# Kernel optimization log

Hardware: AMD Instinct MI355X
Metric: run time of the kernel (lower is better)

## Reference

```python
import jax, jax.numpy as jnp
import numpy as np

T, B, D, H = 110, 256, 512, 512
EPS = 1e-9


def _forward(a, v, l, qmask, umask, mu_a, mu_v, mu_l, shifta, shiftv,
             turna, turnb, W1, b1, W2, b2):
    Tcur = a.shape[0]
    # ca = mu * (cos(a) + i sin(a)) = mu * exp(i a)
    ca = mu_a[:Tcur] * jnp.exp(1j * a)          # (T,B,D) complex64
    cv = mu_v[:Tcur] * jnp.exp(1j * v)
    cl = mu_l[:Tcur] * jnp.exp(1j * l)
    # phase shift of a and v streams, then sum into lav
    features = cl + ca * jnp.exp(1j * shifta) + cv * jnp.exp(1j * shiftv)  # (T,B,D)

    # --- step 0 (special-cased in the original loop) ---
    temp0 = features[0]                          # (B,D) complex
    qa0 = qmask[0][:, 0:1]                       # (B,1)
    qb0 = qmask[0][:, 1:2]
    ones = jnp.ones_like(temp0) * (1.0 + 1.0j)   # pA=pB=1+1j initial state
    pA0 = (1.0 - qa0) * ones + qa0 * temp0
    pB0 = (1.0 - qb0) * ones + qb0 * temp0

    # --- steps 1..T-1 as a fused scan over time ---
    def step(carry, xs):
        pA, pB = carry
        f, qm, ta, tb = xs                       # f:(B,D) cplx, qm:(B,2), ta/tb:(1,D)
        qa = qm[:, 0:1]
        qb = qm[:, 1:2]
        turn = qa * (pA * jnp.exp(1j * ta)) + qb * (pB * jnp.exp(1j * tb))
        # torch: turn.where(turn==0, turn/(abs+eps)) -> keep 0 where 0, else normalize
        turn = jnp.where(turn == 0, turn, turn / (jnp.abs(turn) + EPS))
        temp = f + turn
        pA = (1.0 - qa) * pA + qa * temp
        pB = (1.0 - qb) * pB + qb * temp
        return (pA, pB), temp

    (_, _), temps = jax.lax.scan(
        step, (pA0, pB0),
        (features[1:], qmask[1:], turna[1:Tcur], turnb[1:Tcur]))

    feats = jnp.concatenate([temp0[None], temps], axis=0)  # (T,B,D) complex
    fr, fi = feats.real, feats.imag
    f1r = fr @ W1.T + b1
    f1i = fi @ W1.T + b1
    f2r = fr @ W2.T + b2
    f2i = fi @ W2.T + b2
    xr = f1r - f2i
    xi = f1i + f2r
    return xr + xi                               # (T,B,H) float32


def setup_inputs() -> dict:
    key = jax.random.key(0)
    ks = jax.random.split(key, 12)
    a = jax.random.normal(ks[0], (T, B, D), jnp.float32)
    v = jax.random.normal(ks[1], (T, B, D), jnp.float32)
    l = jax.random.normal(ks[2], (T, B, D), jnp.float32)
    spk = jax.random.randint(ks[3], (T, B), 0, 2)
    qmask = jax.nn.one_hot(spk, 2, dtype=jnp.float32)      # (T,B,2)
    umask = jnp.ones((T, B), jnp.float32)                  # unused by forward
    mu_a = jnp.ones((110, 1, 1), jnp.float32)
    mu_v = jnp.ones((110, 1, 1), jnp.float32)
    mu_l = jnp.ones((110, 1, 1), jnp.float32)
    shifta = jax.random.normal(ks[4], (1, 1, D), jnp.float32)
    shiftv = jax.random.normal(ks[5], (1, 1, D), jnp.float32)
    turna = jax.random.uniform(ks[6], (110, 1, D), jnp.float32)
    turnb = jax.random.uniform(ks[7], (110, 1, D), jnp.float32)
    W1 = jax.random.normal(ks[8], (H, D), jnp.float32) * 0.02
    b1 = jnp.zeros((H,), jnp.float32)
    W2 = jax.random.normal(ks[9], (H, D), jnp.float32) * 0.02
    b2 = jnp.zeros((H,), jnp.float32)
    return {"a": a, "v": v, "l": l, "qmask": qmask, "umask": umask,
            "mu_a": mu_a, "mu_v": mu_v, "mu_l": mu_l,
            "shifta": shifta, "shiftv": shiftv,
            "turna": turna, "turnb": turnb,
            "W1": W1, "b1": b1, "W2": W2, "b2": b2,
            "dia_len": T}


def reference(a, v, l, qmask, umask, mu_a, mu_v, mu_l, shifta, shiftv,
              turna, turnb, W1, b1, W2, b2, dia_len):
    return _forward(a, v, l, qmask, umask, mu_a, mu_v, mu_l,
                    shifta, shiftv, turna, turnb, W1, b1, W2, b2)
```

## Files before the change

### kernel.cpp

```cpp
#include <hip/hip_runtime.h>

#define T_DIM 110
#define B_DIM 256
#define D_DIM 512
#define H_DIM 512
#define K_CAT 1024
#define M_DIM (T_DIM * B_DIM)
#define BD    (B_DIM * D_DIM)
#define EPSV 1e-9f

typedef float f32x4 __attribute__((ext_vector_type(4)));
typedef short bf16x8 __attribute__((ext_vector_type(8)));

static __device__ __forceinline__ unsigned short f2bf(float f) {
    unsigned u = __builtin_bit_cast(unsigned, f);
    u += 0x7fffu + ((u >> 16) & 1u);
    return (unsigned short)(u >> 16);
}

__global__ __launch_bounds__(256) void prep_w_kernel(
    const float* __restrict__ W1, const float* __restrict__ b1,
    const float* __restrict__ W2,
    unsigned short* __restrict__ Bt,
    float* __restrict__ bias2)
{
    int i = blockIdx.x * 256 + threadIdx.x;
    if (i < H_DIM) bias2[i] = 2.0f * b1[i];
    if (i >= H_DIM * K_CAT) return;
    int h = i / K_CAT;
    int k = i % K_CAT;
    float w;
    if (k < D_DIM) w = W1[h * D_DIM + k] + W2[h * D_DIM + k];
    else           w = W1[h * D_DIM + k - D_DIM] - W2[h * D_DIM + k - D_DIM];
    Bt[i] = f2bf(w);
}

__global__ __launch_bounds__(256) void feat_scan_kernel(
    const float* __restrict__ a, const float* __restrict__ v,
    const float* __restrict__ l, const float* __restrict__ qmask,
    const float* __restrict__ mu_a, const float* __restrict__ mu_v,
    const float* __restrict__ mu_l,
    const float* __restrict__ shifta, const float* __restrict__ shiftv,
    const float* __restrict__ turna, const float* __restrict__ turnb,
    unsigned short* __restrict__ A)
{
    const int tid = blockIdx.x * blockDim.x + threadIdx.x;
    const int b = tid >> 9;
    const int d = tid & 511;
    const float sa = shifta[d];
    const float sv = shiftv[d];

    float a0,v0,l0,ta0,tb0,q0,ma0,mv0,ml0;
    float a1,v1,l1,ta1,tb1,q1,ma1,mv1,ml1;
    float a2,v2,l2,ta2,tb2,q2,ma2,mv2,ml2;

#define LOAD_INTO(A_,V_,L_,TA_,TB_,Q_,MA_,MV_,ML_, T_)                        \
    {                                                                          \
        const int t_ = (T_);                                                   \
        A_  = a[(size_t)t_ * BD + tid];                                        \
        V_  = v[(size_t)t_ * BD + tid];                                        \
        L_  = l[(size_t)t_ * BD + tid];                                        \
        TA_ = turna[t_ * D_DIM + d];                                           \
        TB_ = turnb[t_ * D_DIM + d];                                           \
        Q_  = qmask[(size_t)(t_ * B_DIM + b) * 2];                             \
        MA_ = mu_a[t_]; MV_ = mu_v[t_]; ML_ = mu_l[t_];                        \
    }

    LOAD_INTO(a0,v0,l0,ta0,tb0,q0,ma0,mv0,ml0, 0)
    LOAD_INTO(a1,v1,l1,ta1,tb1,q1,ma1,mv1,ml1, 1)
    LOAD_INTO(a2,v2,l2,ta2,tb2,q2,ma2,mv2,ml2, 2)

    float pAr = 0.f, pAi = 0.f, pBr = 0.f, pBi = 0.f;

    #pragma unroll 3
    for (int t = 0; t < T_DIM; ++t) {
        float an,vn,ln,tan_,tbn,qn,man,mvn,mln;
        const int tp = (t + 3 < T_DIM) ? t + 3 : T_DIM - 1;
        LOAD_INTO(an,vn,ln,tan_,tbn,qn,man,mvn,mln, tp)

        float sA, cA, sV, cV, sL, cL;
        __sincosf(a0 + sa, &sA, &cA);
        __sincosf(v0 + sv, &sV, &cV);
        __sincosf(l0,      &sL, &cL);
        float fr = ml0 * cL + ma0 * cA + mv0 * cV;
        float fi = ml0 * sL + ma0 * sA + mv0 * sV;

        const bool isA = q0 > 0.5f;
        if (t == 0) {
            pAr = isA ? fr : 1.0f;  pAi = isA ? fi : 1.0f;
            pBr = isA ? 1.0f : fr;  pBi = isA ? 1.0f : fi;
        } else {
            float ph = isA ? ta0 : tb0;
            float pr = isA ? pAr : pBr;
            float pi = isA ? pAi : pBi;
            float sp, cp;
            __sincosf(ph, &sp, &cp);
            float tr = pr * cp - pi * sp;
            float ti = pr * sp + pi * cp;
            if (!(tr == 0.0f && ti == 0.0f)) {
                float inv = 1.0f / (sqrtf(tr * tr + ti * ti) + EPSV);
                tr *= inv; ti *= inv;
            }
            fr += tr;
            fi += ti;
            if (isA) { pAr = fr; pAi = fi; } else { pBr = fr; pBi = fi; }
        }

        const size_t row = (size_t)(t * B_DIM + b) * K_CAT;
        A[row + d]         = f2bf(fr);
        A[row + D_DIM + d] = f2bf(fi);

        a0=a1; v0=v1; l0=l1; ta0=ta1; tb0=tb1; q0=q1; ma0=ma1; mv0=mv1; ml0=ml1;
        a1=a2; v1=v2; l1=l2; ta1=ta2; tb1=tb2; q1=q2; ma1=ma2; mv1=mv2; ml1=ml2;
        a2=an; v2=vn; l2=ln; ta2=tan_; tb2=tbn; q2=qn; ma2=man; mv2=mvn; ml2=mln;
    }
#undef LOAD_INTO
}

#define BM 128
#define BN 128
#define BK 32
#define LDS_PAD 40

__global__ __launch_bounds__(256) void gemm_kernel(
    const unsigned short* __restrict__ A,
    const unsigned short* __restrict__ Bt,
    const float* __restrict__ bias2,
    float* __restrict__ C)
{
    __shared__ __align__(16) unsigned short As[BM * LDS_PAD];
    __shared__ __align__(16) unsigned short Bs[BN * LDS_PAD];

    int tid = threadIdx.x;
    int wave = tid >> 6;
    int lane = tid & 63;
    int wr = wave >> 1;
    int wc = wave & 1;
    int m0 = blockIdx.x * BM;
    int n0 = blockIdx.y * BN;
    int lrow = lane & 15;
    int lk8 = (lane >> 4) * 8;

    f32x4 acc[4][4] = {};

    for (int k0 = 0; k0 < K_CAT; k0 += BK) {
        #pragma unroll
        for (int j = 0; j < 2; ++j) {
            int ch = tid + 256 * j;
            int row = ch >> 2;
            int cc = ch & 3;
            const uint4* gA = reinterpret_cast<const uint4*>(
                A + (size_t)(m0 + row) * K_CAT + k0 + cc * 8);
            *reinterpret_cast<uint4*>(&As[row * LDS_PAD + cc * 8]) = *gA;
            const uint4* gB = reinterpret_cast<const uint4*>(
                Bt + (size_t)(n0 + row) * K_CAT + k0 + cc * 8);
            *reinterpret_cast<uint4*>(&Bs[row * LDS_PAD + cc * 8]) = *gB;
        }
        __syncthreads();

        bf16x8 af[4], bfv[4];
        #pragma unroll
        for (int m = 0; m < 4; ++m)
            af[m] = *reinterpret_cast<const bf16x8*>(
                &As[(wr * 64 + m * 16 + lrow) * LDS_PAD + lk8]);
        #pragma unroll
        for (int n = 0; n < 4; ++n)
            bfv[n] = *reinterpret_cast<const bf16x8*>(
                &Bs[(wc * 64 + n * 16 + lrow) * LDS_PAD + lk8]);

        #pragma unroll
        for (int m = 0; m < 4; ++m)
            #pragma unroll
            for (int n = 0; n < 4; ++n)
                acc[m][n] = __builtin_amdgcn_mfma_f32_16x16x32_bf16(
                    af[m], bfv[n], acc[m][n], 0, 0, 0);
        __syncthreads();
    }

    int rbase = m0 + wr * 64 + (lane >> 4) * 4;
    int cbase = n0 + wc * 64;
    #pragma unroll
    for (int n = 0; n < 4; ++n) {
        int col = cbase + n * 16 + lrow;
        float bv = bias2[col];
        #pragma unroll
        for (int m = 0; m < 4; ++m) {
            int row0 = rbase + m * 16;
            #pragma unroll
            for (int r = 0; r < 4; ++r) {
                C[(size_t)(row0 + r) * H_DIM + col] = acc[m][n][r] + bv;
            }
        }
    }
}

extern "C" void kernel_launch(void* const* d_in, const int* in_sizes, int n_in,
                              void* d_out, int out_size, void* d_ws, size_t ws_size,
                              hipStream_t stream) {
    const float* a      = (const float*)d_in[0];
    const float* v      = (const float*)d_in[1];
    const float* l      = (const float*)d_in[2];
    const float* qmask  = (const float*)d_in[3];
    const float* mu_a   = (const float*)d_in[5];
    const float* mu_v   = (const float*)d_in[6];
    const float* mu_l   = (const float*)d_in[7];
    const float* shifta = (const float*)d_in[8];
    const float* shiftv = (const float*)d_in[9];
    const float* turna  = (const float*)d_in[10];
    const float* turnb  = (const float*)d_in[11];
    const float* W1     = (const float*)d_in[12];
    const float* b1     = (const float*)d_in[13];
    const float* W2     = (const float*)d_in[14];
    float* out = (float*)d_out;

    char* ws = (char*)d_ws;
    unsigned short* Afeat = (unsigned short*)ws;
    size_t offB  = (size_t)M_DIM * K_CAT * sizeof(unsigned short);
    unsigned short* Bt = (unsigned short*)(ws + offB);
    size_t offBias = offB + (size_t)H_DIM * K_CAT * sizeof(unsigned short);
    float* bias2 = (float*)(ws + offBias);

    prep_w_kernel<<<(H_DIM * K_CAT + 255) / 256, 256, 0, stream>>>(W1, b1, W2, Bt, bias2);
    feat_scan_kernel<<<(B_DIM * D_DIM) / 256, 256, 0, stream>>>(
        a, v, l, qmask, mu_a, mu_v, mu_l, shifta, shiftv, turna, turnb, Afeat);
    dim3 grid(M_DIM / BM, H_DIM / BN);
    gemm_kernel<<<grid, 256, 0, stream>>>(Afeat, Bt, bias2, out);
}
```

Before: 134.0 us.

## Use direct global-to-LDS loads with BK=64 in GEMM and pin scan prefetch registers

The GEMM now stages A and B tiles with global_load_lds (global memory straight into LDS, skipping VGPRs), doubles BK to 64 and drops the LDS row padding. Each sync now covers two MFMA k-substeps, which halves the barrier count. Empty asm register pins were added in the scan kernel so the compiler keeps the three-step prefetch loads issued early instead of sinking them. The unpadded LDS layout (row stride of 128 bytes) may cause bank conflicts on the fragment reads.

```diff
diff --git a/kernel.cpp b/kernel.cpp
--- a/kernel.cpp
+++ b/kernel.cpp
@@ -65,10 +65,15 @@
         Q_  = qmask[(size_t)(t_ * B_DIM + b) * 2];                             \
         MA_ = mu_a[t_]; MV_ = mu_v[t_]; ML_ = mu_l[t_];                        \
     }
+#define PIN6(A_,V_,L_,TA_,TB_,Q_) \
+    asm volatile("" : "+v"(A_), "+v"(V_), "+v"(L_), "+v"(TA_), "+v"(TB_), "+v"(Q_));
 
     LOAD_INTO(a0,v0,l0,ta0,tb0,q0,ma0,mv0,ml0, 0)
     LOAD_INTO(a1,v1,l1,ta1,tb1,q1,ma1,mv1,ml1, 1)
     LOAD_INTO(a2,v2,l2,ta2,tb2,q2,ma2,mv2,ml2, 2)
+    PIN6(a0,v0,l0,ta0,tb0,q0)
+    PIN6(a1,v1,l1,ta1,tb1,q1)
+    PIN6(a2,v2,l2,ta2,tb2,q2)
 
     float pAr = 0.f, pAi = 0.f, pBr = 0.f, pBi = 0.f;
 
@@ -77,6 +82,7 @@
         float an,vn,ln,tan_,tbn,qn,man,mvn,mln;
         const int tp = (t + 3 < T_DIM) ? t + 3 : T_DIM - 1;
         LOAD_INTO(an,vn,ln,tan_,tbn,qn,man,mvn,mln, tp)
+        PIN6(an,vn,ln,tan_,tbn,qn)
 
         float sA, cA, sV, cV, sL, cL;
         __sincosf(a0 + sa, &sA, &cA);
@@ -115,12 +121,12 @@
         a2=an; v2=vn; l2=ln; ta2=tan_; tb2=tbn; q2=qn; ma2=man; mv2=mvn; ml2=mln;
     }
 #undef LOAD_INTO
+#undef PIN6
 }
 
 #define BM 128
 #define BN 128
-#define BK 32
-#define LDS_PAD 40
+#define BK 64
 
 __global__ __launch_bounds__(256) void gemm_kernel(
     const unsigned short* __restrict__ A,
@@ -128,64 +134,82 @@
     const float* __restrict__ bias2,
     float* __restrict__ C)
 {
-    __shared__ __align__(16) unsigned short As[BM * LDS_PAD];
-    __shared__ __align__(16) unsigned short Bs[BN * LDS_PAD];
-
-    int tid = threadIdx.x;
-    int wave = tid >> 6;
-    int lane = tid & 63;
-    int wr = wave >> 1;
-    int wc = wave & 1;
-    int m0 = blockIdx.x * BM;
-    int n0 = blockIdx.y * BN;
-    int lrow = lane & 15;
-    int lk8 = (lane >> 4) * 8;
+    __shared__ __align__(16) unsigned short As[BM * BK];
+    __shared__ __align__(16) unsigned short Bs[BN * BK];
+
+    const int tid = threadIdx.x;
+    const int wave = tid >> 6;
+    const int lane = tid & 63;
+    const int wr = wave >> 1;
+    const int wc = wave & 1;
+    const int m0 = blockIdx.x * BM;
+    const int n0 = blockIdx.y * BN;
+    const int lrow = lane & 15;
+    const int lk8 = (lane >> 4) * 8;
+
+    const int srow = wave * 32;
+    const int lrow8 = lane >> 3;
+    const int lchunk = lane & 7;
 
     f32x4 acc[4][4] = {};
 
     for (int k0 = 0; k0 < K_CAT; k0 += BK) {
         #pragma unroll
-        for (int j = 0; j < 2; ++j) {
-            int ch = tid + 256 * j;
-            int row = ch >> 2;
-            int cc = ch & 3;
-            const uint4* gA = reinterpret_cast<const uint4*>(
-                A + (size_t)(m0 + row) * K_CAT + k0 + cc * 8);
-            *reinterpret_cast<uint4*>(&As[row * LDS_PAD + cc * 8]) = *gA;
-            const uint4* gB = reinterpret_cast<const uint4*>(
-                Bt + (size_t)(n0 + row) * K_CAT + k0 + cc * 8);
-            *reinterpret_cast<uint4*>(&Bs[row * LDS_PAD + cc * 8]) = *gB;
+        for (int c = 0; c < 4; ++c) {
+            const int row = srow + c * 8 + lrow8;
+            {
+                const unsigned short* gp = A + (size_t)(m0 + row) * K_CAT + k0 + lchunk * 8;
+                unsigned short* lp = As + (srow + c * 8) * BK + lane * 8;
+                __builtin_amdgcn_global_load_lds(
+                    (const __attribute__((address_space(1))) unsigned int*)gp,
+                    (__attribute__((address_space(3))) unsigned int*)lp,
+                    16, 0, 0);
+            }
+            {
+                const unsigned short* gp = Bt + (size_t)(n0 + row) * K_CAT + k0 + lchunk * 8;
+                unsigned short* lp = Bs + (srow + c * 8) * BK + lane * 8;
+                __builtin_amdgcn_global_load_lds(
+                    (const __attribute__((address_space(1))) unsigned int*)gp,
+                    (__attribute__((address_space(3))) unsigned int*)lp,
+                    16, 0, 0);
+            }
         }
         __syncthreads();
 
-        bf16x8 af[4], bfv[4];
+        bf16x8 af[4][2], bfv[4][2];
         #pragma unroll
         for (int m = 0; m < 4; ++m)
-            af[m] = *reinterpret_cast<const bf16x8*>(
-                &As[(wr * 64 + m * 16 + lrow) * LDS_PAD + lk8]);
+            #pragma unroll
+            for (int kk = 0; kk < 2; ++kk)
+                af[m][kk] = *reinterpret_cast<const bf16x8*>(
+                    &As[(wr * 64 + m * 16 + lrow) * BK + kk * 32 + lk8]);
         #pragma unroll
         for (int n = 0; n < 4; ++n)
-            bfv[n] = *reinterpret_cast<const bf16x8*>(
-                &Bs[(wc * 64 + n * 16 + lrow) * LDS_PAD + lk8]);
-
-        #pragma unroll
-        for (int m = 0; m < 4; ++m)
-            #pragma unroll
-            for (int n = 0; n < 4; ++n)
-                acc[m][n] = __builtin_amdgcn_mfma_f32_16x16x32_bf16(
-                    af[m], bfv[n], acc[m][n], 0, 0, 0);
+            #pragma unroll
+            for (int kk = 0; kk < 2; ++kk)
+                bfv[n][kk] = *reinterpret_cast<const bf16x8*>(
+                    &Bs[(wc * 64 + n * 16 + lrow) * BK + kk * 32 + lk8]);
+
+        #pragma unroll
+        for (int kk = 0; kk < 2; ++kk)
+            #pragma unroll
+            for (int m = 0; m < 4; ++m)
+                #pragma unroll
+                for (int n = 0; n < 4; ++n)
+                    acc[m][n] = __builtin_amdgcn_mfma_f32_16x16x32_bf16(
+                        af[m][kk], bfv[n][kk], acc[m][n], 0, 0, 0);
         __syncthreads();
     }
 
-    int rbase = m0 + wr * 64 + (lane >> 4) * 4;
-    int cbase = n0 + wc * 64;
+    const int rbase = m0 + wr * 64 + (lane >> 4) * 4;
+    const int cbase = n0 + wc * 64;
     #pragma unroll
     for (int n = 0; n < 4; ++n) {
-        int col = cbase + n * 16 + lrow;
-        float bv = bias2[col];
+        const int col = cbase + n * 16 + lrow;
+        const float bv = bias2[col];
         #pragma unroll
         for (int m = 0; m < 4; ++m) {
-            int row0 = rbase + m * 16;
+            const int row0 = rbase + m * 16;
             #pragma unroll
             for (int r = 0; r < 4; ++r) {
                 C[(size_t)(row0 + r) * H_DIM + col] = acc[m][n][r] + bv;
```

Result: no change. 136.4 us (+1.7%).
